# Optimization experiments

Hardware: AMD Instinct MI355X
Metric: run time of the kernel (lower is better)

The kernel has to match this reference:

```python
import jax, jax.numpy as jnp
import numpy as np

B, S, D = 16, 4096, 64
N_HASHES, BUCKET_SIZE = 8, 64
TOKEN_SELF_ATTN_VALUE = -50000.0


def setup_inputs() -> dict:
    key = jax.random.key(0)
    k1, k2, k3 = jax.random.split(key, 3)
    qk = jax.random.normal(k1, (B, S, D), jnp.float32)
    v = jax.random.normal(k2, (B, S, D), jnp.float32)
    # random rotations for LSH hashing: (batch, dim, n_hashes, n_buckets//2)
    rotations = jax.random.normal(k3, (B, D, N_HASHES, (S // BUCKET_SIZE) // 2), jnp.float32)
    return {"qk": qk, "v": v, "rotations": rotations}


def _look_one_back(x):
    # concat each chunk with the previous chunk (wrapping): (b, c, n, ...) -> (b, c, 2n, ...)
    return jnp.concatenate([x, jnp.roll(x, 1, axis=1)], axis=2)


def _lsh_attention(qk, v, rotations):
    b, s, d = qk.shape
    n_buckets = s // BUCKET_SIZE
    # --- hash vectors (rehash_each_round=True path) ---
    rotated = jnp.einsum('btf,bfhi->bhti', qk, rotations)          # (b, h, s, nb/2)
    rotated = jnp.concatenate([rotated, -rotated], axis=-1)        # (b, h, s, nb)
    buckets = jnp.argmax(rotated, axis=-1)                          # (b, h, s)
    offsets = (jnp.arange(N_HASHES) * n_buckets)[None, :, None]
    buckets = (buckets + offsets).reshape(b, -1)                    # (b, h*s)
    # --- stable bucket sort of tokens ---
    ticker = jnp.arange(N_HASHES * s)[None, :]
    buckets_and_t = s * buckets + ticker % s
    sticker = jnp.argsort(buckets_and_t, axis=-1)                   # sorted order
    undo_sort = jnp.argsort(sticker, axis=-1)
    st = sticker % s                                                # original token index
    sqk = jnp.take_along_axis(qk, st[..., None], axis=1)            # (b, h*s, d)
    sv = jnp.take_along_axis(v, st[..., None], axis=1)
    chunk_size = N_HASHES * n_buckets
    bq_t = st.reshape(b, chunk_size, -1)                            # (b, c, n)
    bqk = sqk.reshape(b, chunk_size, -1, d)                         # (b, c, n, d)
    bv = sv.reshape(b, chunk_size, -1, d)
    # shared-QK: keys are L2-normalized queries
    norm = jnp.linalg.norm(bqk, axis=-1, keepdims=True)
    bk = bqk / jnp.maximum(norm, 1e-12)
    bk = _look_one_back(bk)                                         # (b, c, 2n, d)
    bvl = _look_one_back(bv)
    bkv_t = _look_one_back(bq_t)                                    # (b, c, 2n)
    dots = jnp.einsum('bhie,bhje->bhij', bqk, bk) * (d ** -0.5)     # (b, c, n, 2n)
    # mask self-attention (token attends to itself only as last resort)
    self_mask = bq_t[:, :, :, None] == bkv_t[:, :, None, :]
    dots = jnp.where(self_mask, TOKEN_SELF_ATTN_VALUE, dots)
    # stable softmax per chunk; keep logsumexp for cross-round combination
    lse = jax.nn.logsumexp(dots, axis=-1, keepdims=True)            # (b, c, n, 1)
    p = jnp.exp(dots - lse)
    bo = jnp.einsum('buij,buje->buie', p, bvl)                      # (b, c, n, d)
    so = bo.reshape(b, -1, d)                                       # (b, h*s, d)
    slogits = lse.reshape(b, -1)                                    # (b, h*s)
    # undo the sort
    o = jnp.take_along_axis(so, undo_sort[..., None], axis=1)
    logits = jnp.take_along_axis(slogits, undo_sort, axis=1)
    o = o.reshape(b, N_HASHES, s, d)
    logits = logits.reshape(b, N_HASHES, s, 1)
    # combine hash rounds weighted by softmax over per-round logsumexp
    probs = jnp.exp(logits - jax.nn.logsumexp(logits, axis=1, keepdims=True))
    return jnp.sum(o * probs, axis=1)                               # (b, s, d)


def reference(qk, v, rotations):
    return _lsh_attention(qk, v, rotations)
```

## Files before the change

### kernel.cpp

```cpp
#include <hip/hip_runtime.h>
#include <math.h>

#define NB_B 16
#define NB_S 4096
#define NB_D 64
#define NB_H 8

#define KSTR 72
#define PSTR 136
#define VSTR 72

typedef _Float16 half_t;
typedef __attribute__((ext_vector_type(2))) _Float16 half2t;
typedef __attribute__((ext_vector_type(4))) _Float16 half4;
typedef __attribute__((ext_vector_type(8))) _Float16 half8;
typedef __attribute__((ext_vector_type(4))) float floatx4;

__global__ __launch_bounds__(256) void prep_kernel(const float* __restrict__ qk,
                                                   const float* __restrict__ v,
                                                   half_t* __restrict__ khat,
                                                   half_t* __restrict__ vh,
                                                   float* __restrict__ norm) {
  int g = blockIdx.x * 256 + threadIdx.x;
  float4 qv = ((const float4*)qk)[g];
  float4 vv = ((const float4*)v)[g];
  float ss = qv.x * qv.x + qv.y * qv.y + qv.z * qv.z + qv.w * qv.w;
  for (int off = 1; off < 16; off <<= 1) ss += __shfl_xor(ss, off);
  float nr = fmaxf(sqrtf(ss), 1e-12f);
  float sc = 1.0f / nr;
  half4 hk = {(half_t)(qv.x * sc), (half_t)(qv.y * sc), (half_t)(qv.z * sc),
              (half_t)(qv.w * sc)};
  half4 hv = {(half_t)vv.x, (half_t)vv.y, (half_t)vv.z, (half_t)vv.w};
  ((half4*)khat)[g] = hk;
  ((half4*)vh)[g] = hv;
  if ((threadIdx.x & 15) == 0) norm[g >> 4] = nr;
}

__global__ __launch_bounds__(256, 1) void hash_kernel(const float* __restrict__ qk,
                                                      const float* __restrict__ rot,
                                                      int* __restrict__ bkt) {
  __shared__ float rotS[64 * 32];
  int tid = threadIdx.x;
  int blk = blockIdx.x;
  int tile = blk & 7;
  int bh = blk >> 3;
  int h = bh & 7, b = bh >> 3;

  for (int i = tid; i < 2048; i += 256) {
    int f = i >> 5, ii = i & 31;
    rotS[i] = rot[(((size_t)b * 64 + f) * 8 + h) * 32 + ii];
  }
  __syncthreads();

  int t0 = (tile << 9) + tid;
  const float* qb = qk + (((size_t)b << 12) << 6);

  float acc[2][32];
#pragma unroll
  for (int tok = 0; tok < 2; tok++)
#pragma unroll
    for (int i = 0; i < 32; i++) acc[tok][i] = 0.f;

#pragma unroll 1
  for (int fc = 0; fc < 8; fc++) {
    float q[2][8];
#pragma unroll
    for (int tok = 0; tok < 2; tok++) {
      const float4* qr =
          (const float4*)(qb + ((size_t)(t0 + (tok << 8)) << 6) + fc * 8);
      *(float4*)(q[tok]) = qr[0];
      *(float4*)(q[tok] + 4) = qr[1];
    }
#pragma unroll
    for (int fi = 0; fi < 8; fi++) {
#pragma unroll
      for (int i4 = 0; i4 < 8; i4++) {
        float4 w = *(const float4*)(rotS + (fc * 8 + fi) * 32 + i4 * 4);
#pragma unroll
        for (int tok = 0; tok < 2; tok++) {
          acc[tok][i4 * 4 + 0] = __fadd_rn(acc[tok][i4 * 4 + 0], __fmul_rn(q[tok][fi], w.x));
          acc[tok][i4 * 4 + 1] = __fadd_rn(acc[tok][i4 * 4 + 1], __fmul_rn(q[tok][fi], w.y));
          acc[tok][i4 * 4 + 2] = __fadd_rn(acc[tok][i4 * 4 + 2], __fmul_rn(q[tok][fi], w.z));
          acc[tok][i4 * 4 + 3] = __fadd_rn(acc[tok][i4 * 4 + 3], __fmul_rn(q[tok][fi], w.w));
        }
      }
    }
  }

#pragma unroll
  for (int tok = 0; tok < 2; tok++) {
    float b1 = acc[tok][0];
    int i1 = 0;
#pragma unroll
    for (int i = 1; i < 32; i++)
      if (acc[tok][i] > b1) { b1 = acc[tok][i]; i1 = i; }
#pragma unroll
    for (int i = 0; i < 32; i++) {
      float x = -acc[tok][i];
      if (x > b1) { b1 = x; i1 = 32 + i; }
    }
    bkt[(((size_t)(b * 8 + h)) << 12) + t0 + (tok << 8)] = i1;
  }
}

__global__ __launch_bounds__(256) void sort_kernel(const int* __restrict__ bkt,
                                                   int* __restrict__ st) {
  __shared__ int lb[4096];
  __shared__ int hist[4096];
  __shared__ int cumoff[64];
  int tid = threadIdx.x;
  int b = blockIdx.x >> 3, h = blockIdx.x & 7;
  const int* gb = bkt + (((size_t)(b * 8 + h)) << 12);
  for (int t = tid; t < 4096; t += 256) lb[t] = gb[t];
  for (int i = tid; i < 4096; i += 256) hist[i] = 0;
  __syncthreads();
  for (int t = tid; t < 4096; t += 256) atomicAdd(&hist[((t >> 6) << 6) | lb[t]], 1);
  __syncthreads();
  if (tid < 64) {
    int run = 0;
    for (int cc = 0; cc < 64; cc++) {
      int x = hist[(cc << 6) | tid];
      hist[(cc << 6) | tid] = run;
      run += x;
    }
    int s = run;
    for (int off = 1; off < 64; off <<= 1) {
      int u = __shfl_up(s, off);
      if (tid >= off) s += u;
    }
    cumoff[tid] = s - run;
  }
  __syncthreads();
  int lane = tid & 63;
  for (int p = 0; p < 16; p++) {
    int t = (p << 8) + tid;
    int vb = lb[t];
    unsigned long long m = 0xFFFFFFFFFFFFFFFFull;
#pragma unroll
    for (int bit = 0; bit < 6; bit++) {
      unsigned long long bl = __ballot((vb >> bit) & 1);
      m &= ((vb >> bit) & 1) ? bl : ~bl;
    }
    int rank = __popcll(m & ((1ull << lane) - 1ull));
    int cpos = cumoff[vb] + hist[((t >> 6) << 6) | vb] + rank;
    st[(((size_t)(b * 8 + h)) << 12) + cpos] = t;
  }
}

#define MASK2 -72134.76f
__global__ __launch_bounds__(256) void chunk_kernel(const half_t* __restrict__ khat,
                                                    const half_t* __restrict__ vh,
                                                    const float* __restrict__ norm,
                                                    const int* __restrict__ st,
                                                    half_t* __restrict__ oh,
                                                    float* __restrict__ lse) {
  __shared__ __align__(16) half_t Ks[128 * KSTR];
  __shared__ __align__(16) half_t Vt0[64 * VSTR];
  __shared__ __align__(16) half_t Vt1[64 * VSTR];
  __shared__ int tk[128];
  __shared__ float normS[64];
  int tid = threadIdx.x;
  int g = blockIdx.x & 511;
  int b = blockIdx.x >> 9;
  int h = g >> 6, c = g & 63;
  int gp = (g + 511) & 511;
  int hp = gp >> 6, cp = gp & 63;
  if (tid < 64) {
    tk[tid] = st[(((size_t)(b * 8 + h)) << 12) + (c << 6) + tid];
  } else if (tid < 128) {
    tk[tid] = st[(((size_t)(b * 8 + hp)) << 12) + (cp << 6) + (tid - 64)];
  }
  __syncthreads();
  if (tid < 64) normS[tid] = norm[(b << 12) + tk[tid]];
  for (int idx = tid; idx < 1024; idx += 256) {
    int row = idx >> 3, fo = idx & 7;
    half8 val = *(const half8*)(khat + (((size_t)(b << 12) + tk[row]) << 6) + fo * 8);
    *(half8*)(Ks + row * KSTR + fo * 8) = val;
  }
  {
    int kp = tid & 31, ch = tid >> 5;
    half8 r0 = *(const half8*)(vh + (((size_t)(b << 12) + tk[2 * kp]) << 6) + ch * 8);
    half8 r1 = *(const half8*)(vh + (((size_t)(b << 12) + tk[2 * kp + 1]) << 6) + ch * 8);
    half8 r2 = *(const half8*)(vh + (((size_t)(b << 12) + tk[64 + 2 * kp]) << 6) + ch * 8);
    half8 r3 = *(const half8*)(vh + (((size_t)(b << 12) + tk[65 + 2 * kp]) << 6) + ch * 8);
#pragma unroll
    for (int j = 0; j < 8; j++) {
      half2t p0 = {r0[j], r1[j]};
      half2t p1 = {r2[j], r3[j]};
      *(half2t*)(Vt0 + (ch * 8 + j) * VSTR + 2 * kp) = p0;
      *(half2t*)(Vt1 + (ch * 8 + j) * VSTR + 2 * kp) = p1;
    }
  }
  __syncthreads();

  int lane = tid & 63, w = tid >> 6;
  int m = lane & 15, quad = lane >> 4;
  half8 afr[2];
#pragma unroll
  for (int ki = 0; ki < 2; ki++)
    afr[ki] = *(const half8*)(Ks + (w * 16 + m) * KSTR + ki * 32 + quad * 8);
  bool c0 = (c == 0);
  float scr[4];
#pragma unroll
  for (int r = 0; r < 4; r++) {
    int rr = w * 16 + quad * 4 + r;
    scr[r] = 0.18033688f * normS[rr];
  }
  int ti[4] = {0, 0, 0, 0};
  if (c0) {
#pragma unroll
    for (int r = 0; r < 4; r++) ti[r] = tk[w * 16 + quad * 4 + r];
  }

  float d[8][4];
#pragma unroll
  for (int nt = 0; nt < 8; nt++) {
    floatx4 acc = {0.f, 0.f, 0.f, 0.f};
#pragma unroll
    for (int ki = 0; ki < 2; ki++) {
      half8 bfr = *(const half8*)(Ks + (nt * 16 + m) * KSTR + ki * 32 + quad * 8);
      acc = __builtin_amdgcn_mfma_f32_16x16x32_f16(afr[ki], bfr, acc, 0, 0, 0);
    }
    if (nt < 4) {
      if (nt == w) {
#pragma unroll
        for (int r = 0; r < 4; r++)
          d[nt][r] = (m == quad * 4 + r) ? MASK2 : acc[r] * scr[r];
      } else {
#pragma unroll
        for (int r = 0; r < 4; r++) d[nt][r] = acc[r] * scr[r];
      }
    } else {
      if (c0) {
        int tj = tk[nt * 16 + m];
#pragma unroll
        for (int r = 0; r < 4; r++)
          d[nt][r] = (ti[r] == tj) ? MASK2 : acc[r] * scr[r];
      } else {
#pragma unroll
        for (int r = 0; r < 4; r++) d[nt][r] = acc[r] * scr[r];
      }
    }
  }

  float mr4[4], lr4[4];
#pragma unroll
  for (int r = 0; r < 4; r++) {
    float mm = d[0][r];
#pragma unroll
    for (int nt = 1; nt < 8; nt++) mm = fmaxf(mm, d[nt][r]);
    for (int off = 1; off < 16; off <<= 1) mm = fmaxf(mm, __shfl_xor(mm, off));
    mr4[r] = mm;
  }
#pragma unroll
  for (int nt = 0; nt < 8; nt++)
#pragma unroll
    for (int r = 0; r < 4; r++)
      d[nt][r] = __builtin_amdgcn_exp2f(d[nt][r] - mr4[r]);
#pragma unroll
  for (int r = 0; r < 4; r++) {
    float ll = 0.f;
#pragma unroll
    for (int nt = 0; nt < 8; nt++) ll += d[nt][r];
    for (int off = 1; off < 16; off <<= 1) ll += __shfl_xor(ll, off);
    lr4[r] = ll;
    if (m == 0) {
      int rr = w * 16 + quad * 4 + r;
      lse[(((size_t)(b * 8 + h)) << 12) + tk[rr]] =
          0.69314718f * (mr4[r] + __builtin_amdgcn_logf(ll));
    }
  }
  __syncthreads();

  half_t* Ps = Ks;
#pragma unroll
  for (int nt = 0; nt < 8; nt++) {
#pragma unroll
    for (int r = 0; r < 4; r++) {
      Ps[(w * 16 + quad * 4 + r) * PSTR + nt * 16 + m] = (half_t)d[nt][r];
    }
  }

  half8 pfr[4];
#pragma unroll
  for (int kk = 0; kk < 4; kk++)
    pfr[kk] = *(const half8*)(Ps + (w * 16 + m) * PSTR + kk * 32 + quad * 8);

  floatx4 accO[4];
#pragma unroll
  for (int dt = 0; dt < 4; dt++) accO[dt] = (floatx4){0.f, 0.f, 0.f, 0.f};

#pragma unroll
  for (int dt = 0; dt < 4; dt++) {
#pragma unroll
    for (int kk = 0; kk < 2; kk++) {
      half8 bfr = *(const half8*)(Vt0 + (dt * 16 + m) * VSTR + kk * 32 + quad * 8);
      accO[dt] = __builtin_amdgcn_mfma_f32_16x16x32_f16(pfr[kk], bfr, accO[dt], 0, 0, 0);
    }
#pragma unroll
    for (int kk = 2; kk < 4; kk++) {
      half8 bfr = *(const half8*)(Vt1 + (dt * 16 + m) * VSTR + (kk - 2) * 32 + quad * 8);
      accO[dt] = __builtin_amdgcn_mfma_f32_16x16x32_f16(pfr[kk], bfr, accO[dt], 0, 0, 0);
    }
  }
  __syncthreads();

  half_t* Ot = Vt0;
#pragma unroll
  for (int r = 0; r < 4; r++) {
    float inv = 1.0f / lr4[r];
#pragma unroll
    for (int dt = 0; dt < 4; dt++) {
      Ot[(w * 16 + quad * 4 + r) * VSTR + dt * 16 + m] = (half_t)(accO[dt][r] * inv);
    }
  }
  __syncthreads();
  for (int idx = tid; idx < 512; idx += 256) {
    int row = idx >> 3, fo = idx & 7;
    half8 val = *(const half8*)(Ot + row * VSTR + fo * 8);
    *(half8*)(oh + ((((size_t)(b * 8 + h)) << 12) + tk[row]) * 64 + fo * 8) = val;
  }
}

__global__ __launch_bounds__(256) void combine_kernel(const half_t* __restrict__ oh,
                                                      const float* __restrict__ lse,
                                                      float* __restrict__ out) {
  int idx = blockIdx.x * 256 + threadIdx.x;
  int do8 = idx & 7;
  int ts = idx >> 3;
  int b = ts >> 12, t = ts & 4095;
  size_t base = ((size_t)b << 15) + t;
  float L[8];
  float m = -3.4e38f;
#pragma unroll
  for (int h = 0; h < 8; h++) {
    L[h] = lse[base + ((size_t)h << 12)];
    m = fmaxf(m, L[h]);
  }
  float s = 0.f;
#pragma unroll
  for (int h = 0; h < 8; h++) s += __expf(L[h] - m);
  float lt = m + __logf(s);
  float acc[8];
#pragma unroll
  for (int j = 0; j < 8; j++) acc[j] = 0.f;
#pragma unroll
  for (int h = 0; h < 8; h++) {
    float wgt = __expf(L[h] - lt);
    half8 o = *(const half8*)(oh + ((base + ((size_t)h << 12)) << 6) + do8 * 8);
#pragma unroll
    for (int j = 0; j < 8; j++) acc[j] += wgt * (float)o[j];
  }
  float* dst = out + ((((size_t)b << 12) + t) << 6) + do8 * 8;
  *(float4*)dst = (float4){acc[0], acc[1], acc[2], acc[3]};
  *(float4*)(dst + 4) = (float4){acc[4], acc[5], acc[6], acc[7]};
}

extern "C" void kernel_launch(void* const* d_in, const int* in_sizes, int n_in,
                              void* d_out, int out_size, void* d_ws, size_t ws_size,
                              hipStream_t stream) {
  const float* qk = (const float*)d_in[0];
  const float* v = (const float*)d_in[1];
  const float* rot = (const float*)d_in[2];
  float* out = (float*)d_out;

  int* bkt = (int*)d_ws;
  int* stp = bkt + NB_B * NB_H * NB_S;
  float* lse = (float*)(stp + NB_B * NB_H * NB_S);
  float* norm = lse + NB_B * NB_H * NB_S;
  half_t* khat = (half_t*)(norm + NB_B * NB_S);
  half_t* vh = khat + (size_t)NB_B * NB_S * NB_D;
  half_t* oh = vh + (size_t)NB_B * NB_S * NB_D;

  prep_kernel<<<NB_B * NB_S * 16 / 256, 256, 0, stream>>>(qk, v, khat, vh, norm);
  hash_kernel<<<NB_B * NB_H * 8, 256, 0, stream>>>(qk, rot, bkt);
  sort_kernel<<<NB_B * NB_H, 256, 0, stream>>>(bkt, stp);
  chunk_kernel<<<NB_B * 512, 256, 0, stream>>>(khat, vh, norm, stp, oh, lse);
  combine_kernel<<<NB_B * NB_S * 8 / 256, 256, 0, stream>>>(oh, lse, out);
}
```

Before: 214.4 us.

## Use packed FP32 math in hashing and write attention output directly to global

```diff
diff --git a/kernel.cpp b/kernel.cpp
--- a/kernel.cpp
+++ b/kernel.cpp
@@ -15,6 +15,7 @@
 typedef __attribute__((ext_vector_type(4))) _Float16 half4;
 typedef __attribute__((ext_vector_type(8))) _Float16 half8;
 typedef __attribute__((ext_vector_type(4))) float floatx4;
+typedef __attribute__((ext_vector_type(2))) float float2v;
 
 __global__ __launch_bounds__(256) void prep_kernel(const float* __restrict__ qk,
                                                    const float* __restrict__ v,
@@ -55,11 +56,11 @@
   int t0 = (tile << 9) + tid;
   const float* qb = qk + (((size_t)b << 12) << 6);
 
-  float acc[2][32];
+  float2v acc2[2][16];
 #pragma unroll
   for (int tok = 0; tok < 2; tok++)
 #pragma unroll
-    for (int i = 0; i < 32; i++) acc[tok][i] = 0.f;
+    for (int i = 0; i < 16; i++) acc2[tok][i] = (float2v){0.f, 0.f};
 
 #pragma unroll 1
   for (int fc = 0; fc < 8; fc++) {
@@ -75,13 +76,21 @@
     for (int fi = 0; fi < 8; fi++) {
 #pragma unroll
       for (int i4 = 0; i4 < 8; i4++) {
-        float4 w = *(const float4*)(rotS + (fc * 8 + fi) * 32 + i4 * 4);
+        float4 wv = *(const float4*)(rotS + (fc * 8 + fi) * 32 + i4 * 4);
+        float2v w0 = {wv.x, wv.y};
+        float2v w1 = {wv.z, wv.w};
 #pragma unroll
         for (int tok = 0; tok < 2; tok++) {
-          acc[tok][i4 * 4 + 0] = __fadd_rn(acc[tok][i4 * 4 + 0], __fmul_rn(q[tok][fi], w.x));
-          acc[tok][i4 * 4 + 1] = __fadd_rn(acc[tok][i4 * 4 + 1], __fmul_rn(q[tok][fi], w.y));
-          acc[tok][i4 * 4 + 2] = __fadd_rn(acc[tok][i4 * 4 + 2], __fmul_rn(q[tok][fi], w.z));
-          acc[tok][i4 * 4 + 3] = __fadd_rn(acc[tok][i4 * 4 + 3], __fmul_rn(q[tok][fi], w.w));
+          float2v q2 = {q[tok][fi], q[tok][fi]};
+          float2v p0, p1;
+          asm("v_pk_mul_f32 %0, %2, %3\n\t"
+              "v_pk_add_f32 %1, %1, %0"
+              : "=&v"(p0), "+v"(acc2[tok][i4 * 2])
+              : "v"(q2), "v"(w0));
+          asm("v_pk_mul_f32 %0, %2, %3\n\t"
+              "v_pk_add_f32 %1, %1, %0"
+              : "=&v"(p1), "+v"(acc2[tok][i4 * 2 + 1])
+              : "v"(q2), "v"(w1));
         }
       }
     }
@@ -89,14 +98,20 @@
 
 #pragma unroll
   for (int tok = 0; tok < 2; tok++) {
-    float b1 = acc[tok][0];
+    float a[32];
+#pragma unroll
+    for (int p = 0; p < 16; p++) {
+      a[2 * p] = acc2[tok][p].x;
+      a[2 * p + 1] = acc2[tok][p].y;
+    }
+    float b1 = a[0];
     int i1 = 0;
 #pragma unroll
     for (int i = 1; i < 32; i++)
-      if (acc[tok][i] > b1) { b1 = acc[tok][i]; i1 = i; }
+      if (a[i] > b1) { b1 = a[i]; i1 = i; }
 #pragma unroll
     for (int i = 0; i < 32; i++) {
-      float x = -acc[tok][i];
+      float x = -a[i];
       if (x > b1) { b1 = x; i1 = 32 + i; }
     }
     bkt[(((size_t)(b * 8 + h)) << 12) + t0 + (tok << 8)] = i1;
@@ -303,22 +318,19 @@
       accO[dt] = __builtin_amdgcn_mfma_f32_16x16x32_f16(pfr[kk], bfr, accO[dt], 0, 0, 0);
     }
   }
-  __syncthreads();
-
-  half_t* Ot = Vt0;
+
+  size_t obase = ((size_t)(b * 8 + h)) << 12;
+  float inv[4];
+#pragma unroll
+  for (int r = 0; r < 4; r++) inv[r] = 1.0f / lr4[r];
 #pragma unroll
   for (int r = 0; r < 4; r++) {
-    float inv = 1.0f / lr4[r];
+    int row = w * 16 + quad * 4 + r;
+    size_t rb = (obase + tk[row]) << 6;
 #pragma unroll
     for (int dt = 0; dt < 4; dt++) {
-      Ot[(w * 16 + quad * 4 + r) * VSTR + dt * 16 + m] = (half_t)(accO[dt][r] * inv);
-    }
-  }
-  __syncthreads();
-  for (int idx = tid; idx < 512; idx += 256) {
-    int row = idx >> 3, fo = idx & 7;
-    half8 val = *(const half8*)(Ot + row * VSTR + fo * 8);
-    *(half8*)(oh + ((((size_t)(b * 8 + h)) << 12) + tk[row]) * 64 + fo * 8) = val;
+      oh[rb + dt * 16 + m] = (half_t)(accO[dt][r] * inv[r]);
+    }
   }
 }
 
```

Result: no change. 215.9 us (+0.7%).
